# Performance work log

Hardware: AMD Instinct MI355X
Metric: run time of the kernel (lower is better)

The kernel has to match this reference:

```python
import jax, jax.numpy as jnp
import numpy as np

N, H, E = 40000, 128, 640000
BN_EPS = 1e-5


def setup_inputs() -> dict:
    key = jax.random.key(0)
    ks = jax.random.split(key, 5)
    x = jax.random.normal(ks[0], (N, H), dtype=jnp.float32)
    edge_index = jax.random.randint(ks[1], (2, E), 0, N, dtype=jnp.int64)
    eps = jnp.zeros((1,), dtype=jnp.float32)
    s = 1.0 / np.sqrt(H)  # torch Linear init scale
    W1 = jax.random.uniform(ks[2], (H, H), jnp.float32, -s, s)
    b1 = jnp.zeros((H,), dtype=jnp.float32)
    W2 = jax.random.uniform(ks[3], (H, H), jnp.float32, -s, s)
    b2 = jnp.zeros((H,), dtype=jnp.float32)
    gamma = jnp.ones((H,), dtype=jnp.float32)
    beta = jnp.zeros((H,), dtype=jnp.float32)
    return {"x": x, "edge_index": edge_index, "eps": eps,
            "W1": W1, "b1": b1, "W2": W2, "b2": b2,
            "gamma": gamma, "beta": beta}


def reference(x, edge_index, eps, W1, b1, W2, b2, gamma, beta):
    src = edge_index[0]
    tgt = edge_index[1]
    # gather source features, scatter-add into target rows: [N, H]
    agg = jax.ops.segment_sum(x[src], tgt, num_segments=x.shape[0])
    out = agg + (1.0 + eps) * x
    # MLP: Linear -> ReLU -> Linear -> BatchNorm1d (train mode) -> ReLU
    h = jax.nn.relu(out @ W1.T + b1)
    h = h @ W2.T + b2
    mean = jnp.mean(h, axis=0)
    var = jnp.mean((h - mean) ** 2, axis=0)  # biased var, as BN uses
    h = (h - mean) * jax.lax.rsqrt(var + BN_EPS) * gamma + beta
    return jax.nn.relu(h)
```

## Files before the change

### kernel.cpp

```cpp
#include <hip/hip_runtime.h>

#define HDIM 128
#define BN_EPS 1e-5f
#define SCAN_BINS 1024
#define NPART 8
#define LSTR 136
#define MROWS 16
#define NREP 8

typedef short short8 __attribute__((ext_vector_type(8)));
typedef float floatx4 __attribute__((ext_vector_type(4)));

__device__ __forceinline__ unsigned short f2b(float f) {
    union { float f; unsigned u; } v; v.f = f;
    unsigned r = v.u + 0x7FFFu + ((v.u >> 16) & 1u);
    return (unsigned short)(r >> 16);
}

__device__ __forceinline__ float b2f(unsigned short b) {
    union { unsigned u; float f; } v; v.u = (unsigned)b << 16;
    return v.f;
}

__global__ __launch_bounds__(256) void prep_kernel(
    const float* __restrict__ x, unsigned short* __restrict__ xB, long n4,
    const float* __restrict__ W1, const float* __restrict__ W2,
    unsigned short* __restrict__ W1B, unsigned short* __restrict__ W2B,
    const int* __restrict__ eidx, int* __restrict__ hist,
    int* __restrict__ rank, int E, int N)
{
    int tid = blockIdx.x * 256 + threadIdx.x;
    int stride = gridDim.x * 256;
    if (blockIdx.x == 0 && threadIdx.x < 32) {
        ushort4 z; z.x = 0; z.y = 0; z.z = 0; z.w = 0;
        ((ushort4*)(xB + (size_t)N * HDIM))[threadIdx.x] = z;
    }
    for (long i = tid; i < n4; i += stride) {
        float4 v = ((const float4*)x)[i];
        ushort4 o;
        o.x = f2b(v.x); o.y = f2b(v.y); o.z = f2b(v.z); o.w = f2b(v.w);
        ((ushort4*)xB)[i] = o;
    }
    for (int i = tid; i < HDIM * HDIM; i += stride) {
        W1B[i] = f2b(W1[i]);
        W2B[i] = f2b(W2[i]);
    }
    int E4 = E >> 2;
    const int4* tgt4 = (const int4*)(eidx + E);
    for (int e4 = tid; e4 < E4; e4 += stride) {
        int4 t = tgt4[e4];
        int4 r;
        r.x = atomicAdd(&hist[t.x], 1);
        r.y = atomicAdd(&hist[t.y], 1);
        r.z = atomicAdd(&hist[t.z], 1);
        r.w = atomicAdd(&hist[t.w], 1);
        ((int4*)rank)[e4] = r;
    }
    for (int e = E4 * 4 + tid; e < E; e += stride) {
        rank[e] = atomicAdd(&hist[eidx[E + e]], 1);
    }
}

__global__ __launch_bounds__(256) void block_scan_kernel(
    const int* __restrict__ hist, int* __restrict__ offsets,
    int* __restrict__ blockSums, float* __restrict__ statSum, int N)
{
    __shared__ int ts[256];
    int b = blockIdx.x, t = threadIdx.x;
    if (b == 0) {
        for (int i = t; i < 2 * NREP * HDIM; i += 256) statSum[i] = 0.f;
    }
    int base = b * SCAN_BINS + t * 4;
    int4 h = make_int4(0, 0, 0, 0);
    if (base + 3 < N) {
        h = *(const int4*)(hist + base);
    } else {
        if (base + 0 < N) h.x = hist[base + 0];
        if (base + 1 < N) h.y = hist[base + 1];
        if (base + 2 < N) h.z = hist[base + 2];
    }
    int4 p;
    p.x = (h.x + 7) & ~7;
    p.y = (h.y + 7) & ~7;
    p.z = (h.z + 7) & ~7;
    p.w = (h.w + 7) & ~7;
    int s = p.x + p.y + p.z + p.w;
    ts[t] = s;
    __syncthreads();
    for (int off = 1; off < 256; off <<= 1) {
        int v = ts[t];
        int add = (t >= off) ? ts[t - off] : 0;
        __syncthreads();
        ts[t] = v + add;
        __syncthreads();
    }
    int excl = ts[t] - s;
    int4 o;
    o.x = excl;
    o.y = o.x + p.x;
    o.z = o.y + p.y;
    o.w = o.z + p.z;
    if (base + 3 < N) {
        *(int4*)(offsets + base) = o;
    } else {
        if (base + 0 < N) offsets[base + 0] = o.x;
        if (base + 1 < N) offsets[base + 1] = o.y;
        if (base + 2 < N) offsets[base + 2] = o.z;
    }
    if (t == 255) blockSums[b] = ts[255];
}

__global__ __launch_bounds__(256) void scan_finalize_kernel(
    const int* __restrict__ blockSums, int* __restrict__ offsets,
    const int* __restrict__ hist, int* __restrict__ srcSorted, int N, int NB)
{
    __shared__ int ts[256];
    int b = blockIdx.x, t = threadIdx.x;
    ts[t] = (t < NB) ? blockSums[t] : 0;
    __syncthreads();
    for (int off = 1; off < 256; off <<= 1) {
        int v = ts[t];
        int add = (t >= off) ? ts[t - off] : 0;
        __syncthreads();
        ts[t] = v + add;
        __syncthreads();
    }
    int prefix = (b == 0) ? 0 : ts[b - 1];
    if (b == 0 && t == 0) offsets[N] = ts[NB - 1];
    int base = b * SCAN_BINS + t * 4;
    if (base + 3 < N) {
        int4 o = *(int4*)(offsets + base);
        o.x += prefix; o.y += prefix; o.z += prefix; o.w += prefix;
        *(int4*)(offsets + base) = o;
        int4 h = *(const int4*)(hist + base);
        for (int p = o.x + h.x; p < o.x + ((h.x + 7) & ~7); p++) srcSorted[p] = N;
        for (int p = o.y + h.y; p < o.y + ((h.y + 7) & ~7); p++) srcSorted[p] = N;
        for (int p = o.z + h.z; p < o.z + ((h.z + 7) & ~7); p++) srcSorted[p] = N;
        for (int p = o.w + h.w; p < o.w + ((h.w + 7) & ~7); p++) srcSorted[p] = N;
    } else {
        for (int j = 0; j < 4; j++) {
            int i = base + j;
            if (i < N) {
                int o = offsets[i] + prefix;
                offsets[i] = o;
                int h = hist[i];
                for (int p = o + h; p < o + ((h + 7) & ~7); p++) srcSorted[p] = N;
            }
        }
    }
}

__global__ __launch_bounds__(256) void reorder_kernel(
    const int* __restrict__ eidx, const int* __restrict__ offsets,
    const int* __restrict__ rank, int* __restrict__ srcSorted,
    int E, int partSize)
{
    int part = blockIdx.x & (NPART - 1);
    int bi = blockIdx.x >> 3;
    int nb = gridDim.x >> 3;
    int lo = part * partSize;
    int hi = lo + partSize;
    int stride = nb * 256;
    for (int e = bi * 256 + threadIdx.x; e < E; e += stride) {
        int t = eidx[E + e];
        if (t >= lo && t < hi) {
            srcSorted[offsets[t] + rank[e]] = eidx[e];
        }
    }
}

__global__ __launch_bounds__(256, 8) void mega_kernel(
    const float* __restrict__ x, const unsigned short* __restrict__ xB,
    const int* __restrict__ offsets, const int* __restrict__ srcSorted,
    const float* __restrict__ eps,
    const unsigned short* __restrict__ W1B, const float* __restrict__ b1,
    const unsigned short* __restrict__ W2B, const float* __restrict__ b2,
    float* __restrict__ out, float* __restrict__ statSum,
    float* __restrict__ statSqs, int N)
{
    __shared__ unsigned short sA[MROWS * LSTR];
    __shared__ unsigned short sH[MROWS * LSTR];

    int tid = threadIdx.x;
    int rb = blockIdx.x * MROWS;

    float coef = 1.0f + eps[0];
    int tx = tid & 15, ty = tid >> 4;
    int col = tx * 8;
    {
        int row = rb + ty;
        float acc[8] = {0.f, 0.f, 0.f, 0.f, 0.f, 0.f, 0.f, 0.f};
        if (row < N) {
            float4 xv0 = *(const float4*)(x + (size_t)row * HDIM + col);
            float4 xv1 = *(const float4*)(x + (size_t)row * HDIM + col + 4);
            acc[0] = coef * xv0.x; acc[1] = coef * xv0.y;
            acc[2] = coef * xv0.z; acc[3] = coef * xv0.w;
            acc[4] = coef * xv1.x; acc[5] = coef * xv1.y;
            acc[6] = coef * xv1.z; acc[7] = coef * xv1.w;
            int beg = offsets[row];
            int nb = (offsets[row + 1] - beg) >> 3;
            const int4* sp = (const int4*)(srcSorted + beg);
            int4 ia, ib;
            if (nb > 0) { ia = sp[0]; ib = sp[1]; }
            for (int b = 0; b < nb; b++) {
                short8 u[8];
                u[0] = *(const short8*)(xB + (size_t)ia.x * HDIM + col);
                u[1] = *(const short8*)(xB + (size_t)ia.y * HDIM + col);
                u[2] = *(const short8*)(xB + (size_t)ia.z * HDIM + col);
                u[3] = *(const short8*)(xB + (size_t)ia.w * HDIM + col);
                u[4] = *(const short8*)(xB + (size_t)ib.x * HDIM + col);
                u[5] = *(const short8*)(xB + (size_t)ib.y * HDIM + col);
                u[6] = *(const short8*)(xB + (size_t)ib.z * HDIM + col);
                u[7] = *(const short8*)(xB + (size_t)ib.w * HDIM + col);
                sp += 2;
                if (b + 1 < nb) { ia = sp[0]; ib = sp[1]; }
                #pragma unroll
                for (int q = 0; q < 8; q++)
                    #pragma unroll
                    for (int j = 0; j < 8; j++)
                        acc[j] += b2f((unsigned short)u[q][j]);
            }
        }
        short8 o;
        #pragma unroll
        for (int j = 0; j < 8; j++) o[j] = (short)f2b(acc[j]);
        *(short8*)(sA + ty * LSTR + col) = o;
    }
    __syncthreads();

    int w = tid >> 6;
    int l = tid & 63;
    int m = l & 15, quad = l >> 4;
    int cbase = w * 32;

    floatx4 acc1[2];
    #pragma unroll
    for (int t = 0; t < 2; t++) acc1[t] = (floatx4){0.f, 0.f, 0.f, 0.f};
    #pragma unroll
    for (int kk = 0; kk < 4; kk++) {
        int k0 = kk * 32 + quad * 8;
        short8 a = *(const short8*)(sA + m * LSTR + k0);
        #pragma unroll
        for (int t = 0; t < 2; t++) {
            short8 bfr = *(const short8*)(W1B + (size_t)(cbase + t * 16 + m) * HDIM + k0);
            acc1[t] = __builtin_amdgcn_mfma_f32_16x16x32_bf16(a, bfr, acc1[t], 0, 0, 0);
        }
    }
    #pragma unroll
    for (int t = 0; t < 2; t++) {
        int colc = cbase + t * 16 + m;
        float bs = b1[colc];
        #pragma unroll
        for (int r = 0; r < 4; r++) {
            float v = fmaxf(acc1[t][r] + bs, 0.f);
            sH[(quad * 4 + r) * LSTR + colc] = f2b(v);
        }
    }
    __syncthreads();

    floatx4 acc2[2];
    #pragma unroll
    for (int t = 0; t < 2; t++) acc2[t] = (floatx4){0.f, 0.f, 0.f, 0.f};
    #pragma unroll
    for (int kk = 0; kk < 4; kk++) {
        int k0 = kk * 32 + quad * 8;
        short8 a = *(const short8*)(sH + m * LSTR + k0);
        #pragma unroll
        for (int t = 0; t < 2; t++) {
            short8 bfr = *(const short8*)(W2B + (size_t)(cbase + t * 16 + m) * HDIM + k0);
            acc2[t] = __builtin_amdgcn_mfma_f32_16x16x32_bf16(a, bfr, acc2[t], 0, 0, 0);
        }
    }
    float* repSum = statSum + (blockIdx.x & (NREP - 1)) * HDIM;
    float* repSqs = statSqs + (blockIdx.x & (NREP - 1)) * HDIM;
    int row0 = rb + quad * 4;
    #pragma unroll
    for (int t = 0; t < 2; t++) {
        int colc = cbase + t * 16 + m;
        float bs = b2[colc];
        float cs = 0.f, cq = 0.f;
        #pragma unroll
        for (int r = 0; r < 4; r++) {
            int row = row0 + r;
            if (row < N) {
                float v = acc2[t][r] + bs;
                out[(size_t)row * HDIM + colc] = v;
                cs += v; cq += v * v;
            }
        }
        cs += __shfl_xor(cs, 16, 64);
        cs += __shfl_xor(cs, 32, 64);
        cq += __shfl_xor(cq, 16, 64);
        cq += __shfl_xor(cq, 32, 64);
        if (quad == 0) {
            atomicAdd(&repSum[colc], cs);
            atomicAdd(&repSqs[colc], cq);
        }
    }
}

__global__ __launch_bounds__(256) void bn_apply_kernel(
    float* __restrict__ out, const float* __restrict__ statSum,
    const float* __restrict__ statSqs, const float* __restrict__ gamma,
    const float* __restrict__ beta, int N, long n4)
{
    __shared__ float sSc[HDIM];
    __shared__ float sSh[HDIM];
    int t = threadIdx.x;
    if (t < HDIM) {
        float s = 0.f, q = 0.f;
        #pragma unroll
        for (int r = 0; r < NREP; r++) {
            s += statSum[r * HDIM + t];
            q += statSqs[r * HDIM + t];
        }
        float invN = 1.0f / (float)N;
        float mean = s * invN;
        float var = q * invN - mean * mean;
        float sc = gamma[t] * rsqrtf(var + BN_EPS);
        sSc[t] = sc;
        sSh[t] = beta[t] - mean * sc;
    }
    __syncthreads();
    long stride = (long)gridDim.x * 256;
    for (long i = (long)blockIdx.x * 256 + t; i < n4; i += stride) {
        int cg = (int)(i & 31) * 4;
        float4 v = ((float4*)out)[i];
        v.x = fmaxf(v.x * sSc[cg + 0] + sSh[cg + 0], 0.f);
        v.y = fmaxf(v.y * sSc[cg + 1] + sSh[cg + 1], 0.f);
        v.z = fmaxf(v.z * sSc[cg + 2] + sSh[cg + 2], 0.f);
        v.w = fmaxf(v.w * sSc[cg + 3] + sSh[cg + 3], 0.f);
        ((float4*)out)[i] = v;
    }
}

extern "C" void kernel_launch(void* const* d_in, const int* in_sizes, int n_in,
                              void* d_out, int out_size, void* d_ws, size_t ws_size,
                              hipStream_t stream) {
    const float* x     = (const float*)d_in[0];
    const int*   eidx  = (const int*)d_in[1];
    const float* eps   = (const float*)d_in[2];
    const float* W1    = (const float*)d_in[3];
    const float* b1    = (const float*)d_in[4];
    const float* W2    = (const float*)d_in[5];
    const float* b2    = (const float*)d_in[6];
    const float* gamma = (const float*)d_in[7];
    const float* beta  = (const float*)d_in[8];
    float* out = (float*)d_out;

    int N = in_sizes[0] / HDIM;
    int E = in_sizes[1] / 2;
    size_t NH = (size_t)N * HDIM;
    int NB = (N + SCAN_BINS - 1) / SCAN_BINS;
    int NpadOff = (N + 1 + 3) & ~3;
    int partSize = (N + NPART - 1) / NPART;
    long n4 = (long)NH / 4;
    int Emax = E + 7 * N + 64;

    unsigned short* xB   = (unsigned short*)d_ws;
    unsigned short* W1B  = xB + NH + HDIM;
    unsigned short* W2B  = W1B + HDIM * HDIM;
    float* statSum = (float*)(W2B + HDIM * HDIM);
    float* statSqs = statSum + NREP * HDIM;
    int*   hist    = (int*)(statSqs + NREP * HDIM);
    int*   offsets = hist + N;
    int*   rank    = offsets + NpadOff;
    int*   srcSorted = rank + E;
    int*   blockSums = srcSorted + Emax;

    hipMemsetAsync(hist, 0, (size_t)N * sizeof(int), stream);
    prep_kernel<<<1280, 256, 0, stream>>>(x, xB, n4, W1, W2, W1B, W2B, eidx, hist, rank, E, N);
    block_scan_kernel<<<NB, 256, 0, stream>>>(hist, offsets, blockSums, statSum, N);
    scan_finalize_kernel<<<NB, 256, 0, stream>>>(blockSums, offsets, hist, srcSorted, N, NB);
    reorder_kernel<<<2048, 256, 0, stream>>>(eidx, offsets, rank, srcSorted, E, partSize);
    int gblocks = (N + MROWS - 1) / MROWS;
    mega_kernel<<<gblocks, 256, 0, stream>>>(
        x, xB, offsets, srcSorted, eps, W1B, b1, W2B, b2,
        out, statSum, statSqs, N);
    bn_apply_kernel<<<2048, 256, 0, stream>>>(
        out, statSum, statSqs, gamma, beta, N, n4);
}
```

Measured before the change: 177.0 us.

## Bucket edges by target and source tile, single-pass reorder

The edge histogram now keys on (target, source quarter), so each row's neighbor list is grouped by source-index tile. The aim is better cache locality in the bf16 feature gather. The reorder kernel drops its 8-way target partitioning and scatters every edge in one pass over the edge list. The cost is a scan four times larger, and each sub-bin is padded to a multiple of 8 on its own. That can add many dummy gathers per row when the average degree is about 16.

```diff
diff --git a/kernel.cpp b/kernel.cpp
--- a/kernel.cpp
+++ b/kernel.cpp
@@ -3,7 +3,7 @@
 #define HDIM 128
 #define BN_EPS 1e-5f
 #define SCAN_BINS 1024
-#define NPART 8
+#define NT 4
 #define LSTR 136
 #define MROWS 16
 #define NREP 8
@@ -20,6 +20,10 @@
 __device__ __forceinline__ float b2f(unsigned short b) {
     union { unsigned u; float f; } v; v.u = (unsigned)b << 16;
     return v.f;
+}
+
+__device__ __forceinline__ int ptile(int s, int TS) {
+    return (s >= TS) + (s >= 2 * TS) + (s >= 3 * TS);
 }
 
 __global__ __launch_bounds__(256) void prep_kernel(
@@ -27,7 +31,7 @@
     const float* __restrict__ W1, const float* __restrict__ W2,
     unsigned short* __restrict__ W1B, unsigned short* __restrict__ W2B,
     const int* __restrict__ eidx, int* __restrict__ hist,
-    int* __restrict__ rank, int E, int N)
+    int* __restrict__ rank, int E, int N, int TS)
 {
     int tid = blockIdx.x * 256 + threadIdx.x;
     int stride = gridDim.x * 256;
@@ -46,24 +50,26 @@
         W2B[i] = f2b(W2[i]);
     }
     int E4 = E >> 2;
+    const int4* src4 = (const int4*)eidx;
     const int4* tgt4 = (const int4*)(eidx + E);
     for (int e4 = tid; e4 < E4; e4 += stride) {
         int4 t = tgt4[e4];
+        int4 s = src4[e4];
         int4 r;
-        r.x = atomicAdd(&hist[t.x], 1);
-        r.y = atomicAdd(&hist[t.y], 1);
-        r.z = atomicAdd(&hist[t.z], 1);
-        r.w = atomicAdd(&hist[t.w], 1);
+        r.x = atomicAdd(&hist[(t.x << 2) + ptile(s.x, TS)], 1);
+        r.y = atomicAdd(&hist[(t.y << 2) + ptile(s.y, TS)], 1);
+        r.z = atomicAdd(&hist[(t.z << 2) + ptile(s.z, TS)], 1);
+        r.w = atomicAdd(&hist[(t.w << 2) + ptile(s.w, TS)], 1);
         ((int4*)rank)[e4] = r;
     }
     for (int e = E4 * 4 + tid; e < E; e += stride) {
-        rank[e] = atomicAdd(&hist[eidx[E + e]], 1);
+        rank[e] = atomicAdd(&hist[(eidx[E + e] << 2) + ptile(eidx[e], TS)], 1);
     }
 }
 
 __global__ __launch_bounds__(256) void block_scan_kernel(
     const int* __restrict__ hist, int* __restrict__ offsets,
-    int* __restrict__ blockSums, float* __restrict__ statSum, int N)
+    int* __restrict__ blockSums, float* __restrict__ statSum, int M)
 {
     __shared__ int ts[256];
     int b = blockIdx.x, t = threadIdx.x;
@@ -72,12 +78,12 @@
     }
     int base = b * SCAN_BINS + t * 4;
     int4 h = make_int4(0, 0, 0, 0);
-    if (base + 3 < N) {
+    if (base + 3 < M) {
         h = *(const int4*)(hist + base);
     } else {
-        if (base + 0 < N) h.x = hist[base + 0];
-        if (base + 1 < N) h.y = hist[base + 1];
-        if (base + 2 < N) h.z = hist[base + 2];
+        if (base + 0 < M) h.x = hist[base + 0];
+        if (base + 1 < M) h.y = hist[base + 1];
+        if (base + 2 < M) h.z = hist[base + 2];
     }
     int4 p;
     p.x = (h.x + 7) & ~7;
@@ -100,19 +106,20 @@
     o.y = o.x + p.x;
     o.z = o.y + p.y;
     o.w = o.z + p.z;
-    if (base + 3 < N) {
+    if (base + 3 < M) {
         *(int4*)(offsets + base) = o;
     } else {
-        if (base + 0 < N) offsets[base + 0] = o.x;
-        if (base + 1 < N) offsets[base + 1] = o.y;
-        if (base + 2 < N) offsets[base + 2] = o.z;
+        if (base + 0 < M) offsets[base + 0] = o.x;
+        if (base + 1 < M) offsets[base + 1] = o.y;
+        if (base + 2 < M) offsets[base + 2] = o.z;
     }
     if (t == 255) blockSums[b] = ts[255];
 }
 
 __global__ __launch_bounds__(256) void scan_finalize_kernel(
     const int* __restrict__ blockSums, int* __restrict__ offsets,
-    const int* __restrict__ hist, int* __restrict__ srcSorted, int N, int NB)
+    const int* __restrict__ hist, int* __restrict__ srcSorted,
+    int M, int NB, int N)
 {
     __shared__ int ts[256];
     int b = blockIdx.x, t = threadIdx.x;
@@ -126,9 +133,9 @@
         __syncthreads();
     }
     int prefix = (b == 0) ? 0 : ts[b - 1];
-    if (b == 0 && t == 0) offsets[N] = ts[NB - 1];
+    if (b == 0 && t == 0) offsets[M] = ts[NB - 1];
     int base = b * SCAN_BINS + t * 4;
-    if (base + 3 < N) {
+    if (base + 3 < M) {
         int4 o = *(int4*)(offsets + base);
         o.x += prefix; o.y += prefix; o.z += prefix; o.w += prefix;
         *(int4*)(offsets + base) = o;
@@ -140,7 +147,7 @@
     } else {
         for (int j = 0; j < 4; j++) {
             int i = base + j;
-            if (i < N) {
+            if (i < M) {
                 int o = offsets[i] + prefix;
                 offsets[i] = o;
                 int h = hist[i];
@@ -153,19 +160,13 @@
 __global__ __launch_bounds__(256) void reorder_kernel(
     const int* __restrict__ eidx, const int* __restrict__ offsets,
     const int* __restrict__ rank, int* __restrict__ srcSorted,
-    int E, int partSize)
-{
-    int part = blockIdx.x & (NPART - 1);
-    int bi = blockIdx.x >> 3;
-    int nb = gridDim.x >> 3;
-    int lo = part * partSize;
-    int hi = lo + partSize;
-    int stride = nb * 256;
-    for (int e = bi * 256 + threadIdx.x; e < E; e += stride) {
+    int E, int TS)
+{
+    int stride = gridDim.x * 256;
+    for (int e = blockIdx.x * 256 + threadIdx.x; e < E; e += stride) {
+        int s = eidx[e];
         int t = eidx[E + e];
-        if (t >= lo && t < hi) {
-            srcSorted[offsets[t] + rank[e]] = eidx[e];
-        }
+        srcSorted[offsets[(t << 2) + ptile(s, TS)] + rank[e]] = s;
     }
 }
 
@@ -197,8 +198,9 @@
             acc[2] = coef * xv0.z; acc[3] = coef * xv0.w;
             acc[4] = coef * xv1.x; acc[5] = coef * xv1.y;
             acc[6] = coef * xv1.z; acc[7] = coef * xv1.w;
-            int beg = offsets[row];
-            int nb = (offsets[row + 1] - beg) >> 3;
+            int beg = offsets[row << 2];
+            int end = offsets[(row << 2) + 4];
+            int nb = (end - beg) >> 3;
             const int4* sp = (const int4*)(srcSorted + beg);
             int4 ia, ib;
             if (nb > 0) { ia = sp[0]; ib = sp[1]; }
@@ -351,11 +353,12 @@
     int N = in_sizes[0] / HDIM;
     int E = in_sizes[1] / 2;
     size_t NH = (size_t)N * HDIM;
-    int NB = (N + SCAN_BINS - 1) / SCAN_BINS;
-    int NpadOff = (N + 1 + 3) & ~3;
-    int partSize = (N + NPART - 1) / NPART;
+    int TS = (N + NT - 1) / NT;
+    int M  = N * NT;
+    int NB = (M + SCAN_BINS - 1) / SCAN_BINS;
+    int MpadOff = (M + 1 + 3) & ~3;
     long n4 = (long)NH / 4;
-    int Emax = E + 7 * N + 64;
+    int Emax = E + 7 * M + 64;
 
     unsigned short* xB   = (unsigned short*)d_ws;
     unsigned short* W1B  = xB + NH + HDIM;
@@ -363,16 +366,16 @@
     float* statSum = (float*)(W2B + HDIM * HDIM);
     float* statSqs = statSum + NREP * HDIM;
     int*   hist    = (int*)(statSqs + NREP * HDIM);
-    int*   offsets = hist + N;
-    int*   rank    = offsets + NpadOff;
+    int*   offsets = hist + M;
+    int*   rank    = offsets + MpadOff;
     int*   srcSorted = rank + E;
     int*   blockSums = srcSorted + Emax;
 
-    hipMemsetAsync(hist, 0, (size_t)N * sizeof(int), stream);
-    prep_kernel<<<1280, 256, 0, stream>>>(x, xB, n4, W1, W2, W1B, W2B, eidx, hist, rank, E, N);
-    block_scan_kernel<<<NB, 256, 0, stream>>>(hist, offsets, blockSums, statSum, N);
-    scan_finalize_kernel<<<NB, 256, 0, stream>>>(blockSums, offsets, hist, srcSorted, N, NB);
-    reorder_kernel<<<2048, 256, 0, stream>>>(eidx, offsets, rank, srcSorted, E, partSize);
+    hipMemsetAsync(hist, 0, (size_t)M * sizeof(int), stream);
+    prep_kernel<<<1280, 256, 0, stream>>>(x, xB, n4, W1, W2, W1B, W2B, eidx, hist, rank, E, N, TS);
+    block_scan_kernel<<<NB, 256, 0, stream>>>(hist, offsets, blockSums, statSum, M);
+    scan_finalize_kernel<<<NB, 256, 0, stream>>>(blockSums, offsets, hist, srcSorted, M, NB, N);
+    reorder_kernel<<<1024, 256, 0, stream>>>(eidx, offsets, rank, srcSorted, E, TS);
     int gblocks = (N + MROWS - 1) / MROWS;
     mega_kernel<<<gblocks, 256, 0, stream>>>(
         x, xB, offsets, srcSorted, eps, W1B, b1, W2B, b2,
```

Measured after the change: 187.0 us. 1.06x slower.

## Double-buffer neighbor gathers, drop partitioned reorder, read self term from bf16

Applied to the files above, without the earlier changes.

The gather loop in the fused kernel now double-buffers two sets of eight bf16 neighbor rows, so the next batch's loads are issued before the current batch is accumulated. Launch bounds drop to 4 blocks per SM to leave room for the extra registers. The reorder kernel stops running eight partitioned passes over the edges and scatters every edge in a single pass with fewer blocks. The self term (1+eps)*x is read from the bf16 copy instead of fp32 x, which halves that traffic but rounds the self term to bf16.

```diff
diff --git a/kernel.cpp b/kernel.cpp
--- a/kernel.cpp
+++ b/kernel.cpp
@@ -3,7 +3,6 @@
 #define HDIM 128
 #define BN_EPS 1e-5f
 #define SCAN_BINS 1024
-#define NPART 8
 #define LSTR 136
 #define MROWS 16
 #define NREP 8
@@ -152,25 +151,37 @@
 
 __global__ __launch_bounds__(256) void reorder_kernel(
     const int* __restrict__ eidx, const int* __restrict__ offsets,
-    const int* __restrict__ rank, int* __restrict__ srcSorted,
-    int E, int partSize)
-{
-    int part = blockIdx.x & (NPART - 1);
-    int bi = blockIdx.x >> 3;
-    int nb = gridDim.x >> 3;
-    int lo = part * partSize;
-    int hi = lo + partSize;
-    int stride = nb * 256;
-    for (int e = bi * 256 + threadIdx.x; e < E; e += stride) {
+    const int* __restrict__ rank, int* __restrict__ srcSorted, int E)
+{
+    int stride = gridDim.x * 256;
+    for (int e = blockIdx.x * 256 + threadIdx.x; e < E; e += stride) {
         int t = eidx[E + e];
-        if (t >= lo && t < hi) {
-            srcSorted[offsets[t] + rank[e]] = eidx[e];
-        }
-    }
-}
-
-__global__ __launch_bounds__(256, 8) void mega_kernel(
-    const float* __restrict__ x, const unsigned short* __restrict__ xB,
+        srcSorted[offsets[t] + rank[e]] = eidx[e];
+    }
+}
+
+#define GATHER8(U, I0, I1) do { \
+    U[0] = *(const short8*)(xB + (size_t)(I0).x * HDIM + col); \
+    U[1] = *(const short8*)(xB + (size_t)(I0).y * HDIM + col); \
+    U[2] = *(const short8*)(xB + (size_t)(I0).z * HDIM + col); \
+    U[3] = *(const short8*)(xB + (size_t)(I0).w * HDIM + col); \
+    U[4] = *(const short8*)(xB + (size_t)(I1).x * HDIM + col); \
+    U[5] = *(const short8*)(xB + (size_t)(I1).y * HDIM + col); \
+    U[6] = *(const short8*)(xB + (size_t)(I1).z * HDIM + col); \
+    U[7] = *(const short8*)(xB + (size_t)(I1).w * HDIM + col); \
+} while (0)
+
+#define ACCUM8(U) do { \
+    _Pragma("unroll") \
+    for (int q_ = 0; q_ < 8; q_++) { \
+        _Pragma("unroll") \
+        for (int j_ = 0; j_ < 8; j_++) \
+            acc[j_] += b2f((unsigned short)U[q_][j_]); \
+    } \
+} while (0)
+
+__global__ __launch_bounds__(256, 4) void mega_kernel(
+    const unsigned short* __restrict__ xB,
     const int* __restrict__ offsets, const int* __restrict__ srcSorted,
     const float* __restrict__ eps,
     const unsigned short* __restrict__ W1B, const float* __restrict__ b1,
@@ -191,34 +202,33 @@
         int row = rb + ty;
         float acc[8] = {0.f, 0.f, 0.f, 0.f, 0.f, 0.f, 0.f, 0.f};
         if (row < N) {
-            float4 xv0 = *(const float4*)(x + (size_t)row * HDIM + col);
-            float4 xv1 = *(const float4*)(x + (size_t)row * HDIM + col + 4);
-            acc[0] = coef * xv0.x; acc[1] = coef * xv0.y;
-            acc[2] = coef * xv0.z; acc[3] = coef * xv0.w;
-            acc[4] = coef * xv1.x; acc[5] = coef * xv1.y;
-            acc[6] = coef * xv1.z; acc[7] = coef * xv1.w;
+            short8 xv = *(const short8*)(xB + (size_t)row * HDIM + col);
+            #pragma unroll
+            for (int j = 0; j < 8; j++) acc[j] = coef * b2f((unsigned short)xv[j]);
             int beg = offsets[row];
             int nb = (offsets[row + 1] - beg) >> 3;
             const int4* sp = (const int4*)(srcSorted + beg);
-            int4 ia, ib;
-            if (nb > 0) { ia = sp[0]; ib = sp[1]; }
-            for (int b = 0; b < nb; b++) {
-                short8 u[8];
-                u[0] = *(const short8*)(xB + (size_t)ia.x * HDIM + col);
-                u[1] = *(const short8*)(xB + (size_t)ia.y * HDIM + col);
-                u[2] = *(const short8*)(xB + (size_t)ia.z * HDIM + col);
-                u[3] = *(const short8*)(xB + (size_t)ia.w * HDIM + col);
-                u[4] = *(const short8*)(xB + (size_t)ib.x * HDIM + col);
-                u[5] = *(const short8*)(xB + (size_t)ib.y * HDIM + col);
-                u[6] = *(const short8*)(xB + (size_t)ib.z * HDIM + col);
-                u[7] = *(const short8*)(xB + (size_t)ib.w * HDIM + col);
-                sp += 2;
-                if (b + 1 < nb) { ia = sp[0]; ib = sp[1]; }
-                #pragma unroll
-                for (int q = 0; q < 8; q++)
-                    #pragma unroll
-                    for (int j = 0; j < 8; j++)
-                        acc[j] += b2f((unsigned short)u[q][j]);
+            short8 uA[8], uB[8];
+            int4 p0, p1, q0, q1;
+            if (nb > 0) {
+                p0 = sp[0]; p1 = sp[1];
+                GATHER8(uA, p0, p1);
+                if (nb > 1) { q0 = sp[2]; q1 = sp[3]; }
+            }
+            for (int b = 0; b < nb; ) {
+                if (b + 1 < nb) {
+                    GATHER8(uB, q0, q1);
+                    if (b + 2 < nb) { p0 = sp[2 * (b + 2)]; p1 = sp[2 * (b + 2) + 1]; }
+                }
+                ACCUM8(uA);
+                b++;
+                if (b >= nb) break;
+                if (b + 1 < nb) {
+                    GATHER8(uA, p0, p1);
+                    if (b + 2 < nb) { q0 = sp[2 * (b + 2)]; q1 = sp[2 * (b + 2) + 1]; }
+                }
+                ACCUM8(uB);
+                b++;
             }
         }
         short8 o;
@@ -353,7 +363,6 @@
     size_t NH = (size_t)N * HDIM;
     int NB = (N + SCAN_BINS - 1) / SCAN_BINS;
     int NpadOff = (N + 1 + 3) & ~3;
-    int partSize = (N + NPART - 1) / NPART;
     long n4 = (long)NH / 4;
     int Emax = E + 7 * N + 64;
 
@@ -372,10 +381,10 @@
     prep_kernel<<<1280, 256, 0, stream>>>(x, xB, n4, W1, W2, W1B, W2B, eidx, hist, rank, E, N);
     block_scan_kernel<<<NB, 256, 0, stream>>>(hist, offsets, blockSums, statSum, N);
     scan_finalize_kernel<<<NB, 256, 0, stream>>>(blockSums, offsets, hist, srcSorted, N, NB);
-    reorder_kernel<<<2048, 256, 0, stream>>>(eidx, offsets, rank, srcSorted, E, partSize);
+    reorder_kernel<<<1024, 256, 0, stream>>>(eidx, offsets, rank, srcSorted, E);
     int gblocks = (N + MROWS - 1) / MROWS;
     mega_kernel<<<gblocks, 256, 0, stream>>>(
-        x, xB, offsets, srcSorted, eps, W1B, b1, W2B, b2,
+        xB, offsets, srcSorted, eps, W1B, b1, W2B, b2,
         out, statSum, statSqs, N);
     bn_apply_kernel<<<2048, 256, 0, stream>>>(
         out, statSum, statSqs, gamma, beta, N, n4);
```

Result: slower. 182.3 us (+3.0%).

## Split target histogram into 8 sub-histograms and read self term from bf16 copy

Applied to the files above, without the earlier changes.

The edge-target histogram is split into 8 sub-histograms chosen by block index, which spreads atomic contention. Each rank is tagged with its sub-histogram id, and per-node sub-offsets are built in the finalize scan so the reorder pass can place edges. The mega kernel also reads the (1+eps)*x self term from the bf16 copy instead of fp32 x, halving that read but adding rounding error to the self term. In exchange, the scans now read 8x more histogram data and write an extra offs8 array.

```diff
diff --git a/kernel.cpp b/kernel.cpp
--- a/kernel.cpp
+++ b/kernel.cpp
@@ -4,6 +4,7 @@
 #define BN_EPS 1e-5f
 #define SCAN_BINS 1024
 #define NPART 8
+#define NSUB 8
 #define LSTR 136
 #define MROWS 16
 #define NREP 8
@@ -45,19 +46,22 @@
         W1B[i] = f2b(W1[i]);
         W2B[i] = f2b(W2[i]);
     }
+    int sub = blockIdx.x & (NSUB - 1);
+    int subTag = sub << 24;
+    int* myHist = hist + sub * N;
     int E4 = E >> 2;
     const int4* tgt4 = (const int4*)(eidx + E);
     for (int e4 = tid; e4 < E4; e4 += stride) {
         int4 t = tgt4[e4];
         int4 r;
-        r.x = atomicAdd(&hist[t.x], 1);
-        r.y = atomicAdd(&hist[t.y], 1);
-        r.z = atomicAdd(&hist[t.z], 1);
-        r.w = atomicAdd(&hist[t.w], 1);
+        r.x = atomicAdd(&myHist[t.x], 1) | subTag;
+        r.y = atomicAdd(&myHist[t.y], 1) | subTag;
+        r.z = atomicAdd(&myHist[t.z], 1) | subTag;
+        r.w = atomicAdd(&myHist[t.w], 1) | subTag;
         ((int4*)rank)[e4] = r;
     }
     for (int e = E4 * 4 + tid; e < E; e += stride) {
-        rank[e] = atomicAdd(&hist[eidx[E + e]], 1);
+        rank[e] = atomicAdd(&myHist[eidx[E + e]], 1) | subTag;
     }
 }
 
@@ -73,11 +77,18 @@
     int base = b * SCAN_BINS + t * 4;
     int4 h = make_int4(0, 0, 0, 0);
     if (base + 3 < N) {
-        h = *(const int4*)(hist + base);
+        #pragma unroll
+        for (int s = 0; s < NSUB; s++) {
+            int4 c = *(const int4*)(hist + (size_t)s * N + base);
+            h.x += c.x; h.y += c.y; h.z += c.z; h.w += c.w;
+        }
     } else {
-        if (base + 0 < N) h.x = hist[base + 0];
-        if (base + 1 < N) h.y = hist[base + 1];
-        if (base + 2 < N) h.z = hist[base + 2];
+        #pragma unroll
+        for (int s = 0; s < NSUB; s++) {
+            if (base + 0 < N) h.x += hist[(size_t)s * N + base + 0];
+            if (base + 1 < N) h.y += hist[(size_t)s * N + base + 1];
+            if (base + 2 < N) h.z += hist[(size_t)s * N + base + 2];
+        }
     }
     int4 p;
     p.x = (h.x + 7) & ~7;
@@ -112,7 +123,8 @@
 
 __global__ __launch_bounds__(256) void scan_finalize_kernel(
     const int* __restrict__ blockSums, int* __restrict__ offsets,
-    const int* __restrict__ hist, int* __restrict__ srcSorted, int N, int NB)
+    const int* __restrict__ hist, int* __restrict__ offs8,
+    int* __restrict__ srcSorted, int N, int NB)
 {
     __shared__ int ts[256];
     int b = blockIdx.x, t = threadIdx.x;
@@ -128,30 +140,27 @@
     int prefix = (b == 0) ? 0 : ts[b - 1];
     if (b == 0 && t == 0) offsets[N] = ts[NB - 1];
     int base = b * SCAN_BINS + t * 4;
-    if (base + 3 < N) {
-        int4 o = *(int4*)(offsets + base);
-        o.x += prefix; o.y += prefix; o.z += prefix; o.w += prefix;
-        *(int4*)(offsets + base) = o;
-        int4 h = *(const int4*)(hist + base);
-        for (int p = o.x + h.x; p < o.x + ((h.x + 7) & ~7); p++) srcSorted[p] = N;
-        for (int p = o.y + h.y; p < o.y + ((h.y + 7) & ~7); p++) srcSorted[p] = N;
-        for (int p = o.z + h.z; p < o.z + ((h.z + 7) & ~7); p++) srcSorted[p] = N;
-        for (int p = o.w + h.w; p < o.w + ((h.w + 7) & ~7); p++) srcSorted[p] = N;
-    } else {
-        for (int j = 0; j < 4; j++) {
-            int i = base + j;
-            if (i < N) {
-                int o = offsets[i] + prefix;
-                offsets[i] = o;
-                int h = hist[i];
-                for (int p = o + h; p < o + ((h + 7) & ~7); p++) srcSorted[p] = N;
+    #pragma unroll
+    for (int j = 0; j < 4; j++) {
+        int i = base + j;
+        if (i < N) {
+            int o = offsets[i] + prefix;
+            offsets[i] = o;
+            int run = o, tot = 0;
+            #pragma unroll
+            for (int s = 0; s < NSUB; s++) {
+                offs8[((size_t)i << 3) + s] = run;
+                int c = hist[(size_t)s * N + i];
+                run += c; tot += c;
             }
+            int pend = o + ((tot + 7) & ~7);
+            for (int p = run; p < pend; p++) srcSorted[p] = N;
         }
     }
 }
 
 __global__ __launch_bounds__(256) void reorder_kernel(
-    const int* __restrict__ eidx, const int* __restrict__ offsets,
+    const int* __restrict__ eidx, const int* __restrict__ offs8,
     const int* __restrict__ rank, int* __restrict__ srcSorted,
     int E, int partSize)
 {
@@ -164,13 +173,15 @@
     for (int e = bi * 256 + threadIdx.x; e < E; e += stride) {
         int t = eidx[E + e];
         if (t >= lo && t < hi) {
-            srcSorted[offsets[t] + rank[e]] = eidx[e];
+            int pk = rank[e];
+            srcSorted[offs8[((size_t)t << 3) + (pk >> 24)] + (pk & 0xFFFFFF)]
+                = eidx[e];
         }
     }
 }
 
 __global__ __launch_bounds__(256, 8) void mega_kernel(
-    const float* __restrict__ x, const unsigned short* __restrict__ xB,
+    const unsigned short* __restrict__ xB,
     const int* __restrict__ offsets, const int* __restrict__ srcSorted,
     const float* __restrict__ eps,
     const unsigned short* __restrict__ W1B, const float* __restrict__ b1,
@@ -191,12 +202,9 @@
         int row = rb + ty;
         float acc[8] = {0.f, 0.f, 0.f, 0.f, 0.f, 0.f, 0.f, 0.f};
         if (row < N) {
-            float4 xv0 = *(const float4*)(x + (size_t)row * HDIM + col);
-            float4 xv1 = *(const float4*)(x + (size_t)row * HDIM + col + 4);
-            acc[0] = coef * xv0.x; acc[1] = coef * xv0.y;
-            acc[2] = coef * xv0.z; acc[3] = coef * xv0.w;
-            acc[4] = coef * xv1.x; acc[5] = coef * xv1.y;
-            acc[6] = coef * xv1.z; acc[7] = coef * xv1.w;
+            short8 xv = *(const short8*)(xB + (size_t)row * HDIM + col);
+            #pragma unroll
+            for (int j = 0; j < 8; j++) acc[j] = coef * b2f((unsigned short)xv[j]);
             int beg = offsets[row];
             int nb = (offsets[row + 1] - beg) >> 3;
             const int4* sp = (const int4*)(srcSorted + beg);
@@ -363,19 +371,20 @@
     float* statSum = (float*)(W2B + HDIM * HDIM);
     float* statSqs = statSum + NREP * HDIM;
     int*   hist    = (int*)(statSqs + NREP * HDIM);
-    int*   offsets = hist + N;
-    int*   rank    = offsets + NpadOff;
+    int*   offsets = hist + (size_t)NSUB * N;
+    int*   offs8   = offsets + NpadOff;
+    int*   rank    = offs8 + (size_t)NSUB * N;
     int*   srcSorted = rank + E;
     int*   blockSums = srcSorted + Emax;
 
-    hipMemsetAsync(hist, 0, (size_t)N * sizeof(int), stream);
+    hipMemsetAsync(hist, 0, (size_t)NSUB * N * sizeof(int), stream);
     prep_kernel<<<1280, 256, 0, stream>>>(x, xB, n4, W1, W2, W1B, W2B, eidx, hist, rank, E, N);
     block_scan_kernel<<<NB, 256, 0, stream>>>(hist, offsets, blockSums, statSum, N);
-    scan_finalize_kernel<<<NB, 256, 0, stream>>>(blockSums, offsets, hist, srcSorted, N, NB);
-    reorder_kernel<<<2048, 256, 0, stream>>>(eidx, offsets, rank, srcSorted, E, partSize);
+    scan_finalize_kernel<<<NB, 256, 0, stream>>>(blockSums, offsets, hist, offs8, srcSorted, N, NB);
+    reorder_kernel<<<2048, 256, 0, stream>>>(eidx, offs8, rank, srcSorted, E, partSize);
     int gblocks = (N + MROWS - 1) / MROWS;
     mega_kernel<<<gblocks, 256, 0, stream>>>(
-        x, xB, offsets, srcSorted, eps, W1B, b1, W2B, b2,
+        xB, offsets, srcSorted, eps, W1B, b1, W2B, b2,
         out, statSum, statSqs, N);
     bn_apply_kernel<<<2048, 256, 0, stream>>>(
         out, statSum, statSqs, gamma, beta, N, n4);
```

New measurement: 180.9 us. 1.02x slower.
